# Performance work log

Hardware: AMD Instinct MI355X
Metric: run time of the kernel (lower is better)

## Reference

```python
import jax, jax.numpy as jnp
import numpy as np

SPATIAL_SCALE = 0.25
SAMPLE_NUM = 2  # sampling grid per bin (grid_h = grid_w = 2)
PI = 3.14159265358979


def setup_inputs() -> dict:
    key = jax.random.key(0)
    k1, k2, k3, k4, k5, k6 = jax.random.split(key, 6)
    B, C, H, W = 2, 256, 256, 256
    N = 1000
    features = jax.random.normal(k1, (B, C, H, W), dtype=jnp.float32)
    # rois: (batch_idx, cx, cy, w, h, theta) in image coordinates (stride-4 feature -> 1024px image)
    bidx = jax.random.randint(k2, (N, 1), 0, B).astype(jnp.float32)
    cx = jax.random.uniform(k3, (N, 1), minval=0.0, maxval=1024.0)
    cy = jax.random.uniform(k4, (N, 1), minval=0.0, maxval=1024.0)
    wh = jax.random.uniform(k5, (N, 2), minval=16.0, maxval=256.0)
    th = jax.random.uniform(k6, (N, 1), minval=-PI, maxval=PI)
    rois = jnp.concatenate([bidx, cx, cy, wh, th], axis=1)
    return {"features": features, "rois": rois, "out_w": 7, "out_h": 7}


def _roi_align_rotated(features, rois, out_h, out_w, spatial_scale, sample_num):
    B, C, H, W = features.shape
    N = rois.shape[0]
    b = rois[:, 0].astype(jnp.int32)                      # [N]
    cx = rois[:, 1] * spatial_scale
    cy = rois[:, 2] * spatial_scale
    rw = jnp.maximum(rois[:, 3] * spatial_scale, 0.0)
    rh = jnp.maximum(rois[:, 4] * spatial_scale, 0.0)
    theta = rois[:, 5]

    bin_h = rh / out_h                                    # [N]
    bin_w = rw / out_w
    gh = gw = sample_num

    ph = jnp.arange(out_h, dtype=jnp.float32)
    pw = jnp.arange(out_w, dtype=jnp.float32)
    iy = (jnp.arange(gh, dtype=jnp.float32) + 0.5) / gh
    ix = (jnp.arange(gw, dtype=jnp.float32) + 0.5) / gw

    # roi-local sample coordinates (origin at roi center), before rotation
    yy = (-rh / 2.0)[:, None, None] + bin_h[:, None, None] * (ph[None, :, None] + iy[None, None, :])  # [N,PH,GH]
    xx = (-rw / 2.0)[:, None, None] + bin_w[:, None, None] * (pw[None, :, None] + ix[None, None, :])  # [N,PW,GW]

    yyf = yy[:, :, None, :, None]                         # [N,PH,1,GH,1]
    xxf = xx[:, None, :, None, :]                         # [N,1,PW,1,GW]
    cosv = jnp.cos(theta)[:, None, None, None, None]
    sinv = jnp.sin(theta)[:, None, None, None, None]
    # rotate into feature-map coordinates (mmcv/AerialDetection convention)
    y = yyf * cosv - xxf * sinv + cy[:, None, None, None, None]  # [N,PH,PW,GH,GW]
    x = yyf * sinv + xxf * cosv + cx[:, None, None, None, None]

    S = out_h * out_w * gh * gw
    y = y.reshape(N, S)
    x = x.reshape(N, S)

    valid = (y > -1.0) & (y < H) & (x > -1.0) & (x < W)
    yc = jnp.clip(y, 0.0, H - 1.0)
    xc = jnp.clip(x, 0.0, W - 1.0)
    y0 = jnp.floor(yc).astype(jnp.int32)
    x0 = jnp.floor(xc).astype(jnp.int32)
    y0 = jnp.minimum(y0, H - 1)
    x0 = jnp.minimum(x0, W - 1)
    y1 = jnp.minimum(y0 + 1, H - 1)
    x1 = jnp.minimum(x0 + 1, W - 1)
    ly = yc - y0.astype(jnp.float32)
    lx = xc - x0.astype(jnp.float32)
    hy, hx = 1.0 - ly, 1.0 - lx
    vm = valid.astype(features.dtype)
    w00 = (hy * hx * vm)[:, :, None]
    w01 = (hy * lx * vm)[:, :, None]
    w10 = (ly * hx * vm)[:, :, None]
    w11 = (ly * lx * vm)[:, :, None]

    bb = jnp.broadcast_to(b[:, None], (N, S))
    # gathers produce [N, S, C] (advanced indices around the channel slice move to front)
    out = (w00 * features[bb, :, y0, x0]
           + w01 * features[bb, :, y0, x1]
           + w10 * features[bb, :, y1, x0]
           + w11 * features[bb, :, y1, x1])

    count = max(gh * gw, 1)
    out = out.reshape(N, out_h, out_w, gh * gw, C).mean(axis=3) * (gh * gw / count)
    return out.transpose(0, 3, 1, 2)                      # [N, C, out_h, out_w]


def reference(features, rois, out_w, out_h):
    return _roi_align_rotated(features, rois, out_h, out_w, SPATIAL_SCALE, SAMPLE_NUM)
```

## Files before the change

### kernel.cpp

```cpp
#include <hip/hip_runtime.h>
#include <hip/hip_bf16.h>

constexpr int Bc = 2;
constexpr int Cc = 256;
constexpr int Hc = 256;
constexpr int Wc = 256;
constexpr int OH = 7;
constexpr int OW = 7;
constexpr int HW = Hc * Wc;
constexpr float SCALE = 0.25f;
constexpr int PAD = 258;

__device__ inline ushort f2bf(float f) {
  uint u = __builtin_bit_cast(uint, f);
  u += 0x7FFFu + ((u >> 16) & 1u);
  return (ushort)(u >> 16);
}
__device__ inline float bf2f(ushort h) {
  return __builtin_bit_cast(float, ((uint)h) << 16);
}

__global__ __launch_bounds__(256) void transpose_bf16(
    const float* __restrict__ in, ushort* __restrict__ outT) {
  __shared__ ushort lds[64 * PAD];
  const int b   = blockIdx.y;
  const int p0  = blockIdx.x * 64;
  const int tid = threadIdx.x;

  const float* inb  = in   + (size_t)b * Cc * HW;
  ushort*      outb = outT + (size_t)b * HW * Cc;

  const int cg = tid >> 4;
  const int px = (tid & 15) * 4;

#pragma unroll
  for (int k = 0; k < 16; ++k) {
    const int c = k * 16 + cg;
    const float4 v =
        *reinterpret_cast<const float4*>(inb + (size_t)c * HW + p0 + px);
    lds[(px + 0) * PAD + c] = f2bf(v.x);
    lds[(px + 1) * PAD + c] = f2bf(v.y);
    lds[(px + 2) * PAD + c] = f2bf(v.z);
    lds[(px + 3) * PAD + c] = f2bf(v.w);
  }
  __syncthreads();

#pragma unroll
  for (int k = 0; k < 8; ++k) {
    const int ci  = tid + k * 256;
    const int pix = ci >> 5;
    const int c   = (ci & 31) * 8;
    uint4 w;
    w.x = (uint)lds[pix * PAD + c + 0] | ((uint)lds[pix * PAD + c + 1] << 16);
    w.y = (uint)lds[pix * PAD + c + 2] | ((uint)lds[pix * PAD + c + 3] << 16);
    w.z = (uint)lds[pix * PAD + c + 4] | ((uint)lds[pix * PAD + c + 5] << 16);
    w.w = (uint)lds[pix * PAD + c + 6] | ((uint)lds[pix * PAD + c + 7] << 16);
    *reinterpret_cast<uint4*>(outb + (size_t)(p0 + pix) * Cc + c) = w;
  }
}

__global__ __launch_bounds__(256) void roi_gather_bf16(
    const float* __restrict__ rois, const ushort* __restrict__ feat,
    float* __restrict__ out, int N) {
  const int n = blockIdx.x;
  if (n >= N) return;
  const int c = threadIdx.x;

  const float* r = rois + (size_t)n * 6;
  const int   b     = (int)r[0];
  const float cx    = r[1] * SCALE;
  const float cy    = r[2] * SCALE;
  const float rw    = fmaxf(r[3] * SCALE, 0.0f);
  const float rh    = fmaxf(r[4] * SCALE, 0.0f);
  const float theta = r[5];

  float sinv, cosv;
  sincosf(theta, &sinv, &cosv);
  const float bin_h = rh * (1.0f / OH);
  const float bin_w = rw * (1.0f / OW);

  const ushort* fb    = feat + (size_t)b * HW * Cc;
  float*        obase = out + ((size_t)n * Cc + c) * (OH * OW);

  for (int ph = 0; ph < OH; ++ph) {
    float acc[OW];
#pragma unroll
    for (int pw = 0; pw < OW; ++pw) acc[pw] = 0.0f;

#pragma unroll
    for (int pw = 0; pw < OW; ++pw) {
#pragma unroll
      for (int s = 0; s < 4; ++s) {
        const int sy = s >> 1;
        const int sx = s & 1;
        const float yy = -rh * 0.5f + bin_h * ((float)ph + (sy + 0.5f) * 0.5f);
        const float xx = -rw * 0.5f + bin_w * ((float)pw + (sx + 0.5f) * 0.5f);
        const float y = yy * cosv - xx * sinv + cy;
        const float x = yy * sinv + xx * cosv + cx;
        if ((y > -1.0f) & (y < (float)Hc) & (x > -1.0f) & (x < (float)Wc)) {
          const float yc = fminf(fmaxf(y, 0.0f), (float)(Hc - 1));
          const float xc = fminf(fmaxf(x, 0.0f), (float)(Wc - 1));
          int y0 = (int)yc;
          int x0 = (int)xc;
          const int y1 = min(y0 + 1, Hc - 1);
          const int x1 = min(x0 + 1, Wc - 1);
          const float ly = yc - (float)y0;
          const float lx = xc - (float)x0;
          const float hy = 1.0f - ly;
          const float hx = 1.0f - lx;
          const float f00 = bf2f(fb[((size_t)(y0 * Wc + x0)) * Cc + c]);
          const float f01 = bf2f(fb[((size_t)(y0 * Wc + x1)) * Cc + c]);
          const float f10 = bf2f(fb[((size_t)(y1 * Wc + x0)) * Cc + c]);
          const float f11 = bf2f(fb[((size_t)(y1 * Wc + x1)) * Cc + c]);
          acc[pw] += hy * hx * f00 + hy * lx * f01 + ly * hx * f10 + ly * lx * f11;
        }
      }
    }
#pragma unroll
    for (int pw = 0; pw < OW; ++pw) obase[ph * OW + pw] = acc[pw] * 0.25f;
  }
}

__global__ __launch_bounds__(256) void roi_align_nchw_fallback(
    const float* __restrict__ rois, const float* __restrict__ feat,
    float* __restrict__ out) {
  const int n  = blockIdx.x;
  const int ph = blockIdx.y;
  const int c  = threadIdx.x;
  const float* r = rois + (size_t)n * 6;
  const int   b     = (int)r[0];
  const float cx    = r[1] * SCALE;
  const float cy    = r[2] * SCALE;
  const float rw    = fmaxf(r[3] * SCALE, 0.0f);
  const float rh    = fmaxf(r[4] * SCALE, 0.0f);
  const float theta = r[5];
  const float cosv = cosf(theta);
  const float sinv = sinf(theta);
  const float bin_h = rh / OH;
  const float bin_w = rw / OW;
  const float* fb = feat + ((size_t)b * Cc + c) * HW;
  float* orow = out + (((size_t)n * Cc + c) * OH + ph) * OW;
  for (int pw = 0; pw < OW; ++pw) {
    float acc = 0.0f;
#pragma unroll
    for (int s = 0; s < 4; ++s) {
      const int sy = s >> 1;
      const int sx = s & 1;
      const float yy = -rh * 0.5f + bin_h * ((float)ph + (sy + 0.5f) * 0.5f);
      const float xx = -rw * 0.5f + bin_w * ((float)pw + (sx + 0.5f) * 0.5f);
      const float y = yy * cosv - xx * sinv + cy;
      const float x = yy * sinv + xx * cosv + cx;
      if ((y > -1.0f) & (y < (float)Hc) & (x > -1.0f) & (x < (float)Wc)) {
        const float yc = fminf(fmaxf(y, 0.0f), (float)(Hc - 1));
        const float xc = fminf(fmaxf(x, 0.0f), (float)(Wc - 1));
        int y0 = (int)yc;
        int x0 = (int)xc;
        const int y1 = min(y0 + 1, Hc - 1);
        const int x1 = min(x0 + 1, Wc - 1);
        const float ly = yc - (float)y0;
        const float lx = xc - (float)x0;
        const float hy = 1.0f - ly;
        const float hx = 1.0f - lx;
        acc += hy * hx * fb[(size_t)y0 * Wc + x0] +
               hy * lx * fb[(size_t)y0 * Wc + x1] +
               ly * hx * fb[(size_t)y1 * Wc + x0] +
               ly * lx * fb[(size_t)y1 * Wc + x1];
      }
    }
    orow[pw] = acc * 0.25f;
  }
}

extern "C" void kernel_launch(void* const* d_in, const int* in_sizes, int n_in,
                              void* d_out, int out_size, void* d_ws,
                              size_t ws_size, hipStream_t stream) {
  const float* features = (const float*)d_in[0];
  const float* rois     = (const float*)d_in[1];
  float* out = (float*)d_out;
  const int N = in_sizes[1] / 6;

  const size_t needed = (size_t)Bc * HW * Cc * sizeof(ushort);
  if (ws_size >= needed) {
    ushort* featT = (ushort*)d_ws;
    transpose_bf16<<<dim3(HW / 64, Bc), 256, 0, stream>>>(features, featT);
    roi_gather_bf16<<<dim3(N), 256, 0, stream>>>(rois, featT, out, N);
  } else {
    roi_align_nchw_fallback<<<dim3(N, OH), 256, 0, stream>>>(features ? rois : rois, features, out);
  }
}
```

Measured before the change: 336.9 us.

## Pack bf16 pairs in transpose LDS and precompute bilinear tables in gather

The transpose kernel now packs two bf16 channels into one 32-bit LDS word and reads them back with vector loads, which cuts LDS traffic and the number of 16-bit accesses. The gather kernel precomputes per-ROI sample weights and offsets into shared memory once per block, rather than recomputing coordinates in every channel thread. It also runs 512 threads split across output rows to raise parallelism. The cost is an extra barrier and some shared memory, plus an uneven 4/3 row split between the two halves of the block.

```diff
diff --git a/kernel.cpp b/kernel.cpp
--- a/kernel.cpp
+++ b/kernel.cpp
@@ -9,20 +9,23 @@
 constexpr int OW = 7;
 constexpr int HW = Hc * Wc;
 constexpr float SCALE = 0.25f;
-constexpr int PAD = 258;
-
-__device__ inline ushort f2bf(float f) {
+constexpr int LDSW = 130;
+
+__device__ inline uint f2bf_bits(float f) {
   uint u = __builtin_bit_cast(uint, f);
   u += 0x7FFFu + ((u >> 16) & 1u);
-  return (ushort)(u >> 16);
+  return u >> 16;
+}
+__device__ inline uint pack2(float lo, float hi) {
+  return f2bf_bits(lo) | (f2bf_bits(hi) << 16);
 }
 __device__ inline float bf2f(ushort h) {
   return __builtin_bit_cast(float, ((uint)h) << 16);
 }
 
-__global__ __launch_bounds__(256) void transpose_bf16(
+__global__ __launch_bounds__(256) void transpose_pk(
     const float* __restrict__ in, ushort* __restrict__ outT) {
-  __shared__ ushort lds[64 * PAD];
+  __shared__ uint lds[64 * LDSW];
   const int b   = blockIdx.y;
   const int p0  = blockIdx.x * 64;
   const int tid = threadIdx.x;
@@ -34,90 +37,113 @@
   const int px = (tid & 15) * 4;
 
 #pragma unroll
-  for (int k = 0; k < 16; ++k) {
-    const int c = k * 16 + cg;
-    const float4 v =
-        *reinterpret_cast<const float4*>(inb + (size_t)c * HW + p0 + px);
-    lds[(px + 0) * PAD + c] = f2bf(v.x);
-    lds[(px + 1) * PAD + c] = f2bf(v.y);
-    lds[(px + 2) * PAD + c] = f2bf(v.z);
-    lds[(px + 3) * PAD + c] = f2bf(v.w);
+  for (int k = 0; k < 8; ++k) {
+    const int c   = k * 32 + cg * 2;
+    const int col = k * 16 + cg;
+    const float4 a  = *reinterpret_cast<const float4*>(
+        inb + (size_t)c * HW + p0 + px);
+    const float4 bv = *reinterpret_cast<const float4*>(
+        inb + (size_t)(c + 1) * HW + p0 + px);
+    lds[(px + 0) * LDSW + col] = pack2(a.x, bv.x);
+    lds[(px + 1) * LDSW + col] = pack2(a.y, bv.y);
+    lds[(px + 2) * LDSW + col] = pack2(a.z, bv.z);
+    lds[(px + 3) * LDSW + col] = pack2(a.w, bv.w);
   }
   __syncthreads();
 
 #pragma unroll
   for (int k = 0; k < 8; ++k) {
-    const int ci  = tid + k * 256;
+    const int ci  = k * 256 + tid;
     const int pix = ci >> 5;
-    const int c   = (ci & 31) * 8;
+    const int c4  = (ci & 31) * 4;
+    const uint* rp = &lds[pix * LDSW + c4];
+    const uint2 w0 = *reinterpret_cast<const uint2*>(rp);
+    const uint2 w1 = *reinterpret_cast<const uint2*>(rp + 2);
     uint4 w;
-    w.x = (uint)lds[pix * PAD + c + 0] | ((uint)lds[pix * PAD + c + 1] << 16);
-    w.y = (uint)lds[pix * PAD + c + 2] | ((uint)lds[pix * PAD + c + 3] << 16);
-    w.z = (uint)lds[pix * PAD + c + 4] | ((uint)lds[pix * PAD + c + 5] << 16);
-    w.w = (uint)lds[pix * PAD + c + 6] | ((uint)lds[pix * PAD + c + 7] << 16);
-    *reinterpret_cast<uint4*>(outb + (size_t)(p0 + pix) * Cc + c) = w;
-  }
-}
-
-__global__ __launch_bounds__(256) void roi_gather_bf16(
+    w.x = w0.x; w.y = w0.y; w.z = w1.x; w.w = w1.y;
+    *reinterpret_cast<uint4*>(outb + (size_t)(p0 + pix) * Cc + c4 * 2) = w;
+  }
+}
+
+__global__ __launch_bounds__(512) void roi_gather_tab(
     const float* __restrict__ rois, const ushort* __restrict__ feat,
     float* __restrict__ out, int N) {
-  const int n = blockIdx.x;
-  if (n >= N) return;
-  const int c = threadIdx.x;
+  __shared__ float4 twt[OH * OW * 4];
+  __shared__ int4   tof[OH * OW * 4];
+
+  const int n   = blockIdx.x;
+  const int tid = threadIdx.x;
 
   const float* r = rois + (size_t)n * 6;
-  const int   b     = (int)r[0];
-  const float cx    = r[1] * SCALE;
-  const float cy    = r[2] * SCALE;
-  const float rw    = fmaxf(r[3] * SCALE, 0.0f);
-  const float rh    = fmaxf(r[4] * SCALE, 0.0f);
-  const float theta = r[5];
-
-  float sinv, cosv;
-  sincosf(theta, &sinv, &cosv);
-  const float bin_h = rh * (1.0f / OH);
-  const float bin_w = rw * (1.0f / OW);
-
-  const ushort* fb    = feat + (size_t)b * HW * Cc;
-  float*        obase = out + ((size_t)n * Cc + c) * (OH * OW);
-
-  for (int ph = 0; ph < OH; ++ph) {
+  const int bidx = (int)r[0];
+
+  if (tid < OH * OW * 4) {
+    const int s   = tid;
+    const int ph  = s / (OW * 4);
+    const int rem = s % (OW * 4);
+    const int pw  = rem >> 2;
+    const int sy  = (rem >> 1) & 1;
+    const int sx  = rem & 1;
+
+    const float cx    = r[1] * SCALE;
+    const float cy    = r[2] * SCALE;
+    const float rw    = fmaxf(r[3] * SCALE, 0.0f);
+    const float rh    = fmaxf(r[4] * SCALE, 0.0f);
+    const float theta = r[5];
+    float sinv, cosv;
+    sincosf(theta, &sinv, &cosv);
+    const float bin_h = rh * (1.0f / OH);
+    const float bin_w = rw * (1.0f / OW);
+
+    const float yy = -rh * 0.5f + bin_h * ((float)ph + (sy + 0.5f) * 0.5f);
+    const float xx = -rw * 0.5f + bin_w * ((float)pw + (sx + 0.5f) * 0.5f);
+    const float y = yy * cosv - xx * sinv + cy;
+    const float x = yy * sinv + xx * cosv + cx;
+    const bool valid =
+        (y > -1.0f) & (y < (float)Hc) & (x > -1.0f) & (x < (float)Wc);
+
+    const float yc = fminf(fmaxf(y, 0.0f), (float)(Hc - 1));
+    const float xc = fminf(fmaxf(x, 0.0f), (float)(Wc - 1));
+    const int y0 = (int)yc;
+    const int x0 = (int)xc;
+    const int y1 = min(y0 + 1, Hc - 1);
+    const int x1 = min(x0 + 1, Wc - 1);
+    const float ly = yc - (float)y0;
+    const float lx = xc - (float)x0;
+    const float hy = 1.0f - ly;
+    const float hx = 1.0f - lx;
+    const float vm = valid ? 1.0f : 0.0f;
+
+    twt[s] = make_float4(hy * hx * vm, hy * lx * vm, ly * hx * vm, ly * lx * vm);
+    tof[s] = make_int4((y0 * Wc + x0) * Cc, (y0 * Wc + x1) * Cc,
+                       (y1 * Wc + x0) * Cc, (y1 * Wc + x1) * Cc);
+  }
+  __syncthreads();
+
+  const int c = tid & 255;
+  const int h = tid >> 8;
+  const ushort* fb = feat + (size_t)bidx * HW * Cc + c;
+  float* obase = out + ((size_t)n * Cc + c) * (OH * OW);
+
+  const int ph_begin = h ? 4 : 0;
+  const int ph_end   = h ? OH : 4;
+  for (int ph = ph_begin; ph < ph_end; ++ph) {
     float acc[OW];
 #pragma unroll
-    for (int pw = 0; pw < OW; ++pw) acc[pw] = 0.0f;
-
-#pragma unroll
     for (int pw = 0; pw < OW; ++pw) {
-#pragma unroll
-      for (int s = 0; s < 4; ++s) {
-        const int sy = s >> 1;
-        const int sx = s & 1;
-        const float yy = -rh * 0.5f + bin_h * ((float)ph + (sy + 0.5f) * 0.5f);
-        const float xx = -rw * 0.5f + bin_w * ((float)pw + (sx + 0.5f) * 0.5f);
-        const float y = yy * cosv - xx * sinv + cy;
-        const float x = yy * sinv + xx * cosv + cx;
-        if ((y > -1.0f) & (y < (float)Hc) & (x > -1.0f) & (x < (float)Wc)) {
-          const float yc = fminf(fmaxf(y, 0.0f), (float)(Hc - 1));
-          const float xc = fminf(fmaxf(x, 0.0f), (float)(Wc - 1));
-          int y0 = (int)yc;
-          int x0 = (int)xc;
-          const int y1 = min(y0 + 1, Hc - 1);
-          const int x1 = min(x0 + 1, Wc - 1);
-          const float ly = yc - (float)y0;
-          const float lx = xc - (float)x0;
-          const float hy = 1.0f - ly;
-          const float hx = 1.0f - lx;
-          const float f00 = bf2f(fb[((size_t)(y0 * Wc + x0)) * Cc + c]);
-          const float f01 = bf2f(fb[((size_t)(y0 * Wc + x1)) * Cc + c]);
-          const float f10 = bf2f(fb[((size_t)(y1 * Wc + x0)) * Cc + c]);
-          const float f11 = bf2f(fb[((size_t)(y1 * Wc + x1)) * Cc + c]);
-          acc[pw] += hy * hx * f00 + hy * lx * f01 + ly * hx * f10 + ly * lx * f11;
-        }
+      float a = 0.0f;
+#pragma unroll
+      for (int sub = 0; sub < 4; ++sub) {
+        const int i = (ph * OW + pw) * 4 + sub;
+        const float4 w = twt[i];
+        const int4   o = tof[i];
+        a += w.x * bf2f(fb[o.x]) + w.y * bf2f(fb[o.y]) +
+             w.z * bf2f(fb[o.z]) + w.w * bf2f(fb[o.w]);
       }
+      acc[pw] = a * 0.25f;
     }
 #pragma unroll
-    for (int pw = 0; pw < OW; ++pw) obase[ph * OW + pw] = acc[pw] * 0.25f;
+    for (int pw = 0; pw < OW; ++pw) obase[ph * OW + pw] = acc[pw];
   }
 }
 
@@ -153,8 +179,8 @@
       if ((y > -1.0f) & (y < (float)Hc) & (x > -1.0f) & (x < (float)Wc)) {
         const float yc = fminf(fmaxf(y, 0.0f), (float)(Hc - 1));
         const float xc = fminf(fmaxf(x, 0.0f), (float)(Wc - 1));
-        int y0 = (int)yc;
-        int x0 = (int)xc;
+        const int y0 = (int)yc;
+        const int x0 = (int)xc;
         const int y1 = min(y0 + 1, Hc - 1);
         const int x1 = min(x0 + 1, Wc - 1);
         const float ly = yc - (float)y0;
@@ -182,9 +208,9 @@
   const size_t needed = (size_t)Bc * HW * Cc * sizeof(ushort);
   if (ws_size >= needed) {
     ushort* featT = (ushort*)d_ws;
-    transpose_bf16<<<dim3(HW / 64, Bc), 256, 0, stream>>>(features, featT);
-    roi_gather_bf16<<<dim3(N), 256, 0, stream>>>(rois, featT, out, N);
+    transpose_pk<<<dim3(HW / 64, Bc), 256, 0, stream>>>(features, featT);
+    roi_gather_tab<<<dim3(N), 512, 0, stream>>>(rois, featT, out, N);
   } else {
-    roi_align_nchw_fallback<<<dim3(N, OH), 256, 0, stream>>>(features ? rois : rois, features, out);
-  }
-}
+    roi_align_nchw_fallback<<<dim3(N, OH), 256, 0, stream>>>(rois, features, out);
+  }
+}
```

After: 296.4 us. -12.0%, faster.
